# Kernel tuning notes

Hardware: AMD Instinct MI355X
Metric: run time of the kernel (lower is better)

Reference implementation:

```python
import jax, jax.numpy as jnp
import numpy as np

D_MODEL = 768
D_FF = 3072
N_BEHAVIORS = 4
EPS = 1e-12


def layer_norm(x, g, b):
    m = jnp.mean(x, axis=-1, keepdims=True)
    v = jnp.mean(jnp.square(x - m), axis=-1, keepdims=True)
    return (x - m) * jax.lax.rsqrt(v + EPS) * g + b


def setup_inputs() -> dict:
    key = jax.random.key(0)
    ks = jax.random.split(key, 8)
    B, L = 8, 2048
    s1 = 1.0 / np.sqrt(D_MODEL)
    s2 = 1.0 / np.sqrt(D_FF)
    return {
        "input_tensor": jax.random.normal(ks[0], (B, L, D_MODEL), dtype=jnp.float32),
        "type_seq": jax.random.randint(ks[1], (B, L), 0, N_BEHAVIORS + 1),
        # per-behavior FeedForward params, stacked on leading n dim
        "W1": jax.random.normal(ks[2], (N_BEHAVIORS, D_MODEL, D_FF), dtype=jnp.float32) * s1,
        "b1": jnp.zeros((N_BEHAVIORS, D_FF), dtype=jnp.float32),
        "W2": jax.random.normal(ks[3], (N_BEHAVIORS, D_FF, D_MODEL), dtype=jnp.float32) * s2,
        "b2": jnp.zeros((N_BEHAVIORS, D_MODEL), dtype=jnp.float32),
        "ln_g": jnp.ones((N_BEHAVIORS, D_MODEL), dtype=jnp.float32),
        "ln_b": jnp.zeros((N_BEHAVIORS, D_MODEL), dtype=jnp.float32),
        # outer LayerNorm params
        "out_g": jnp.ones((D_MODEL,), dtype=jnp.float32),
        "out_b": jnp.zeros((D_MODEL,), dtype=jnp.float32),
    }


def reference(input_tensor, type_seq, W1, b1, W2, b2, ln_g, ln_b, out_g, out_b):
    n = W1.shape[0]
    # run every behavior's FeedForward over the full sequence (dense over-compute)
    h = jnp.einsum('BLH,nHF->nBLF', input_tensor, W1) + b1[:, None, None, :]
    h = jax.nn.gelu(h, approximate=False)  # torch 'gelu' = exact erf form
    h = jnp.einsum('nBLF,nFH->nBLH', h, W2) + b2[:, None, None, :]
    # per-expert residual LayerNorm (FeedForward with residual=True)
    h = layer_norm(h + input_tensor[None], ln_g[:, None, None, :], ln_b[:, None, None, :])
    # prepend zeros branch (class 0 = padding) then one-hot select per token
    stacked = jnp.concatenate([jnp.zeros_like(input_tensor)[None], h], axis=0)  # [n+1,B,L,H]
    onehot = jax.nn.one_hot(type_seq, n + 1, dtype=input_tensor.dtype)  # [B,L,n+1]
    sel = jnp.einsum('nBLH,BLn->BLH', stacked, onehot)
    # dropout is identity in eval; fused residual + LayerNorm
    return layer_norm(sel + input_tensor, out_g, out_b)
```

## Files before the change

kernel.cpp:

```cpp
#include <hip/hip_runtime.h>
#include <hip/hip_bf16.h>
#include <math.h>

#define NTOK   16384
#define DM     768
#define DF     3072
#define NEXP   4

#define RBLKS  64
#define XBLKS  768
#define WBLKS  288
#define PREP_BLKS (RBLKS + XBLKS + WBLKS)
#define W2BLKS 288

typedef short bf16x8 __attribute__((ext_vector_type(8)));
typedef float f32x4  __attribute__((ext_vector_type(4)));

#define WS_CNT    0u
#define WS_BASES  256u
#define WS_POS    512u
#define WS_LIST   (512u + 65536u)
#define WS_XB     (WS_LIST + 262144u)
#define WS_W1T    (WS_XB + 25165824u)
#define WS_W2T    (WS_W1T + 18874368u)
#define WS_H1     (WS_W2T + 18874368u)
#define WS_H2     (WS_H1 + 100663296u)
#define WS_END    (WS_H2 + 25165824u)

__device__ __forceinline__ ushort f2bf(float f) {
    unsigned int v; __builtin_memcpy(&v, &f, 4);
    v = v + 0x7fffu + ((v >> 16) & 1u);
    return (ushort)(v >> 16);
}
__device__ __forceinline__ float bf2f(ushort u) {
    unsigned int v = ((unsigned int)u) << 16;
    float f; __builtin_memcpy(&f, &v, 4); return f;
}

__device__ __forceinline__ float fast_gelu(float v) {
    float y = v + 0.044715f * v * v * v;
    float e = __builtin_amdgcn_exp2f(-2.3022082f * y);
    return v * __builtin_amdgcn_rcpf(1.0f + e);
}

typedef __attribute__((address_space(1))) const void gvoid_t;
typedef __attribute__((address_space(3))) void lvoid_t;
__device__ __forceinline__ void cp16(const void* g, void* l) {
    __builtin_amdgcn_global_load_lds((gvoid_t*)g, (lvoid_t*)l, 16, 0, 0);
}

__device__ __forceinline__ int xcd_remap(int id, int T) {
    const int q = T >> 3, r = T & 7;
    const int x = id & 7, j = id >> 3;
    return (x < r ? x * (q + 1) : r * (q + 1) + (x - r) * q) + j;
}

__global__ __launch_bounds__(256) void prep_kernel(
    const int* __restrict__ type_seq, const float* __restrict__ X,
    const float* __restrict__ W1,
    int* __restrict__ cnt,
    int* __restrict__ pos_of, int* __restrict__ list,
    ushort* __restrict__ Xb, ushort* __restrict__ W1t) {
    __shared__ ushort tbuf[2][64 * 72];
    __shared__ int lcnt[NEXP];
    __shared__ int lbase[NEXP];
    const int tid = threadIdx.x;
    const int bid = blockIdx.x;

    if (bid < RBLKS) {
        if (tid < NEXP) lcnt[tid] = 0;
        __syncthreads();
        const int lane = tid & 63;
        const int t = bid * 256 + tid;
        const int k = type_seq[t];
        int my_e = -1, my_p = 0;
#pragma unroll
        for (int e = 0; e < NEXP; ++e) {
            unsigned long long m = __ballot(k == e + 1);
            int total = __popcll(m);
            int b = 0;
            if (lane == 0 && total) b = atomicAdd(&lcnt[e], total);
            b = __shfl(b, 0, 64);
            if (k == e + 1) {
                my_e = e;
                my_p = b + __popcll(m & ((1ull << lane) - 1ull));
            }
        }
        __syncthreads();
        if (tid < NEXP && lcnt[tid] > 0)
            lbase[tid] = atomicAdd(&cnt[tid], lcnt[tid]);
        __syncthreads();
        if (my_e >= 0) {
            int gp = lbase[my_e] + my_p;
            list[my_e * NTOK + gp] = t;
            pos_of[t] = gp;
        }
        return;
    }

    int id = bid - RBLKS;
    if (id < XBLKS) {
        size_t ibase = ((size_t)id * 8 * 256 + tid) * 8;
        float4 va[8], vb[8];
#pragma unroll
        for (int k = 0; k < 8; ++k) {
            va[k] = *(const float4*)(X + ibase + (size_t)k * 2048);
            vb[k] = *(const float4*)(X + ibase + (size_t)k * 2048 + 4);
        }
#pragma unroll
        for (int k = 0; k < 8; ++k) {
            ushort tmp[8];
            tmp[0] = f2bf(va[k].x); tmp[1] = f2bf(va[k].y);
            tmp[2] = f2bf(va[k].z); tmp[3] = f2bf(va[k].w);
            tmp[4] = f2bf(vb[k].x); tmp[5] = f2bf(vb[k].y);
            tmp[6] = f2bf(vb[k].z); tmp[7] = f2bf(vb[k].w);
            *(uint4*)(Xb + ibase + (size_t)k * 2048) = *(uint4*)tmp;
        }
        return;
    }
    id -= XBLKS;
    {
        const int lr = tid >> 3;
        const int lc = (tid & 7) * 8;
        float4 v[2][2];
        const int base_tt = id * 8;
        auto LOADT = [&](int tt) {
            int z = tt / 576, rr = tt % 576, bx = rr % 48, by = rr / 48;
            const float* s0 = W1 + (size_t)z * DM * DF + (size_t)(by * 64 + lr) * DF + bx * 64 + lc;
            v[0][0] = *(const float4*)s0;       v[0][1] = *(const float4*)(s0 + 4);
            const float* s1 = s0 + (size_t)32 * DF;
            v[1][0] = *(const float4*)s1;       v[1][1] = *(const float4*)(s1 + 4);
        };
        LOADT(base_tt);
#pragma unroll 1
        for (int k = 0; k < 8; ++k) {
            ushort* tb = &tbuf[k & 1][0];
#pragma unroll
            for (int q = 0; q < 2; ++q) {
                int r = lr + q * 32;
                ushort tmp[8];
                tmp[0] = f2bf(v[q][0].x); tmp[1] = f2bf(v[q][0].y);
                tmp[2] = f2bf(v[q][0].z); tmp[3] = f2bf(v[q][0].w);
                tmp[4] = f2bf(v[q][1].x); tmp[5] = f2bf(v[q][1].y);
                tmp[6] = f2bf(v[q][1].z); tmp[7] = f2bf(v[q][1].w);
                int sw = (((lc >> 3) ^ ((r >> 3) & 7)) << 3);
                *(uint4*)&tb[r * 72 + sw] = *(uint4*)tmp;
            }
            if (k < 7) LOADT(base_tt + k + 1);
            __syncthreads();
            int tt = base_tt + k;
            int z = tt / 576, rr = tt % 576, bx = rr % 48, by = rr / 48;
#pragma unroll
            for (int q = 0; q < 2; ++q) {
                int r = lr + q * 32;
                ushort tmp[8];
#pragma unroll
                for (int j = 0; j < 8; ++j)
                    tmp[j] = tb[(lc + j) * 72 +
                                ((((r >> 3) & 7) ^ (((lc + j) >> 3) & 7)) << 3) + (r & 7)];
                *(uint4*)(W1t + (size_t)z * DM * DF + (size_t)(bx * 64 + r) * DM + by * 64 + lc) = *(uint4*)tmp;
            }
        }
    }
}

__global__ __launch_bounds__(512, 4) void gemm1_kernel(
    const ushort* __restrict__ Xb, const ushort* __restrict__ W1t,
    const float* __restrict__ b1, const int* __restrict__ cnt,
    const int* __restrict__ list, ushort* __restrict__ h1,
    const float* __restrict__ W2, ushort* __restrict__ W2t) {
    __shared__ __align__(16) short As[3][4096];
    __shared__ __align__(16) short Bs[3][4096];
    const int tid = threadIdx.x;

    const int c0 = cnt[0], c1 = cnt[1], c2 = cnt[2], c3 = cnt[3];
    const int p0 = (c0 + 127) >> 7, p1 = (c1 + 127) >> 7, p2 = (c2 + 127) >> 7;
    const int mb = p0 + p1 + p2 + ((c3 + 127) >> 7);
    const int T = mb * 24;
    int id = blockIdx.y * 24 + blockIdx.x;

    if (id >= T) {
        int wid = id - T;
        if (wid >= W2BLKS) return;
        ushort* tb = (ushort*)&As[0][0];
        const int lr = tid >> 3;
        const int lc = (tid & 7) * 8;
#pragma unroll 1
        for (int k = 0; k < 8; ++k) {
            int tt = wid * 8 + k;
            int zz = tt / 576, rr = tt % 576, bx = rr % 12, by = rr / 12;
            size_t mbase = (size_t)zz * DM * DF;
            const float* s = W2 + mbase + (size_t)(by * 64 + lr) * DM + bx * 64 + lc;
            float4 v0 = *(const float4*)s;
            float4 v1 = *(const float4*)(s + 4);
            ushort tmp[8];
            tmp[0] = f2bf(v0.x); tmp[1] = f2bf(v0.y); tmp[2] = f2bf(v0.z); tmp[3] = f2bf(v0.w);
            tmp[4] = f2bf(v1.x); tmp[5] = f2bf(v1.y); tmp[6] = f2bf(v1.z); tmp[7] = f2bf(v1.w);
            int sw = (((lc >> 3) ^ ((lr >> 3) & 7)) << 3);
            __syncthreads();
            *(uint4*)&tb[lr * 72 + sw] = *(uint4*)tmp;
            __syncthreads();
            ushort o[8];
#pragma unroll
            for (int j = 0; j < 8; ++j)
                o[j] = tb[(lc + j) * 72 +
                          ((((lr >> 3) & 7) ^ (((lc + j) >> 3) & 7)) << 3) + (lr & 7)];
            *(uint4*)(W2t + mbase + (size_t)(bx * 64 + lr) * DF + by * 64 + lc) = *(uint4*)o;
        }
        return;
    }

    id = xcd_remap(id, T);
    const int y = id / 24;
    const int n0 = (id % 24) * 128;
    const int q1 = p0, q2 = p0 + p1, q3 = p0 + p1 + p2;
    const int e = (y >= q1) + (y >= q2) + (y >= q3);
    const int mstart = (e > 0) * p0 + (e > 1) * p1 + (e > 2) * p2;
    const int m0 = (y - mstart) << 7;
    const int count = (e == 0) ? c0 : ((e == 1) ? c1 : ((e == 2) ? c2 : c3));
    const int base = (e > 0) * c0 + (e > 1) * c1 + (e > 2) * c2;
    const int NK = DM / 32;

    const int wave = tid >> 6, lane = tid & 63;
    const int wm = (wave & 1) * 64, wn = (wave >> 1) * 32;
    const int lrow = lane & 15;
    const int qg = lane >> 4;

    int r0 = min(m0 + (tid >> 2), count - 1);
    int t0 = list[e * NTOK + r0];
    const int qsrc = ((tid & 3) ^ ((tid >> 3) & 3)) * 8;
    const ushort* a0 = Xb + (size_t)t0 * DM + qsrc;
    const ushort* Wb = W1t + (size_t)e * DF * DM;
    const ushort* bp0 = Wb + (size_t)(n0 + (tid >> 2)) * DM + qsrc;

    int aOff[4], bOff[2];
#pragma unroll
    for (int i = 0; i < 4; ++i) {
        int ra = wm + i * 16 + lrow;
        aOff[i] = ra * 32 + (qg ^ ((ra >> 1) & 3)) * 8;
    }
#pragma unroll
    for (int j = 0; j < 2; ++j) {
        int rb = wn + j * 16 + lrow;
        bOff[j] = rb * 32 + (qg ^ ((rb >> 1) & 3)) * 8;
    }

    f32x4 z = {0.f, 0.f, 0.f, 0.f};
    f32x4 acc[4][2];
#pragma unroll
    for (int i = 0; i < 4; ++i)
#pragma unroll
        for (int j = 0; j < 2; ++j) acc[i][j] = z;

    auto STAGE = [&](int wb) {
        cp16(a0, &As[0][0] + wb * 4096 + tid * 8);
        cp16(bp0, &Bs[0][0] + wb * 4096 + tid * 8);
        a0 += 32; bp0 += 32;
    };

    STAGE(0); STAGE(1);
    int rb = 0;
    for (int ks = 0; ks < NK; ++ks) {
        __builtin_amdgcn_sched_barrier(0);
        if (ks + 1 < NK) { asm volatile("s_waitcnt vmcnt(2)" ::: "memory"); }
        else             { asm volatile("s_waitcnt vmcnt(0)" ::: "memory"); }
        __builtin_amdgcn_s_barrier();
        __builtin_amdgcn_sched_barrier(0);
        if (ks + 2 < NK) {
            int wb = rb - 1; if (wb < 0) wb += 3;
            STAGE(wb);
        }
        const short* Ab = &As[0][0] + rb * 4096;
        const short* Bb = &Bs[0][0] + rb * 4096;
        bf16x8 av[4], bv[2];
#pragma unroll
        for (int i = 0; i < 4; ++i) av[i] = *(const bf16x8*)(Ab + aOff[i]);
#pragma unroll
        for (int j = 0; j < 2; ++j) bv[j] = *(const bf16x8*)(Bb + bOff[j]);
#pragma unroll
        for (int i = 0; i < 4; ++i)
#pragma unroll
            for (int j = 0; j < 2; ++j)
                acc[i][j] = __builtin_amdgcn_mfma_f32_16x16x32_bf16(av[i], bv[j], acc[i][j], 0, 0, 0);
        rb = (rb + 1 == 3) ? 0 : rb + 1;
    }

    float bias[2];
#pragma unroll
    for (int nt = 0; nt < 2; ++nt)
        bias[nt] = b1[e * DF + n0 + wn + nt * 16 + lrow];
#pragma unroll
    for (int mt = 0; mt < 4; ++mt) {
        int gm = m0 + wm + mt * 16 + (lane >> 4) * 4;
#pragma unroll
        for (int nt = 0; nt < 2; ++nt) {
            int gn = n0 + wn + nt * 16 + lrow;
#pragma unroll
            for (int r = 0; r < 4; ++r) {
                int i = gm + r;
                if (i < count) {
                    float v = acc[mt][nt][r] + bias[nt];
                    h1[(size_t)(base + i) * DF + gn] = f2bf(fast_gelu(v));
                }
            }
        }
    }
}

__global__ __launch_bounds__(256, 3) void gemm2_kernel(
    const ushort* __restrict__ h1, const ushort* __restrict__ W2t,
    const float* __restrict__ b2, const int* __restrict__ cnt,
    ushort* __restrict__ h2) {
    const int c0 = cnt[0], c1 = cnt[1], c2 = cnt[2], c3 = cnt[3];
    const int p0 = (c0 + 127) >> 7, p1 = (c1 + 127) >> 7, p2 = (c2 + 127) >> 7;
    const int mb = p0 + p1 + p2 + ((c3 + 127) >> 7);
    const int T = mb * 6;
    int id = blockIdx.y * 6 + blockIdx.x;
    if (id >= T) return;
    id = xcd_remap(id, T);
    const int y = id / 6;
    const int n0 = (id % 6) * 128;
    const int q1 = p0, q2 = p0 + p1, q3 = p0 + p1 + p2;
    const int e = (y >= q1) + (y >= q2) + (y >= q3);
    const int mstart = (e > 0) * p0 + (e > 1) * p1 + (e > 2) * p2;
    const int m0 = (y - mstart) << 7;
    const int count = (e == 0) ? c0 : ((e == 1) ? c1 : ((e == 2) ? c2 : c3));
    const int base = (e > 0) * c0 + (e > 1) * c1 + (e > 2) * c2;
    const int NK = DF / 32;

    __shared__ __align__(16) short As[3][4096];
    __shared__ __align__(16) short Bs[3][4096];

    const int tid = threadIdx.x;
    const int wave = tid >> 6, lane = tid & 63;
    const int wm = (wave & 1) * 64, wn = (wave >> 1) * 64;
    const int lrow = lane & 15;
    const int qg = lane >> 4;

    const int srow = tid >> 2;
    const int qsrc = ((tid & 3) ^ ((tid >> 3) & 3)) * 8;
    int r0 = min(m0 + srow, count - 1);
    int r1 = min(m0 + 64 + srow, count - 1);
    const ushort* a0 = h1 + (size_t)(base + r0) * DF + qsrc;
    const ushort* a1 = h1 + (size_t)(base + r1) * DF + qsrc;
    const ushort* Wb = W2t + (size_t)e * DM * DF;
    const ushort* bp0 = Wb + (size_t)(n0 + srow) * DF + qsrc;
    const ushort* bp1 = bp0 + (size_t)64 * DF;

    int aOff[4], bOff[4];
#pragma unroll
    for (int i = 0; i < 4; ++i) {
        int ra = wm + i * 16 + lrow;
        aOff[i] = ra * 32 + (qg ^ ((ra >> 1) & 3)) * 8;
        int rbo = wn + i * 16 + lrow;
        bOff[i] = rbo * 32 + (qg ^ ((rbo >> 1) & 3)) * 8;
    }

    f32x4 z = {0.f, 0.f, 0.f, 0.f};
    f32x4 acc[4][4];
#pragma unroll
    for (int i = 0; i < 4; ++i)
#pragma unroll
        for (int j = 0; j < 4; ++j) acc[i][j] = z;

    auto STAGE = [&](int wb) {
        cp16(a0, &As[wb][0] + tid * 8);
        cp16(a1, &As[wb][2048] + tid * 8);
        cp16(bp0, &Bs[wb][0] + tid * 8);
        cp16(bp1, &Bs[wb][2048] + tid * 8);
        a0 += 32; a1 += 32; bp0 += 32; bp1 += 32;
    };

    STAGE(0); STAGE(1);
    int rb = 0;
    for (int ks = 0; ks < NK; ++ks) {
        __builtin_amdgcn_sched_barrier(0);
        if (ks + 1 < NK) { asm volatile("s_waitcnt vmcnt(4)" ::: "memory"); }
        else             { asm volatile("s_waitcnt vmcnt(0)" ::: "memory"); }
        __builtin_amdgcn_s_barrier();
        __builtin_amdgcn_sched_barrier(0);
        if (ks + 2 < NK) {
            int wb = rb - 1; if (wb < 0) wb += 3;
            STAGE(wb);
        }
        const short* Ab = &As[rb][0];
        const short* Bb = &Bs[rb][0];
        bf16x8 av[4], bv[4];
#pragma unroll
        for (int i = 0; i < 4; ++i) av[i] = *(const bf16x8*)(Ab + aOff[i]);
#pragma unroll
        for (int j = 0; j < 4; ++j) bv[j] = *(const bf16x8*)(Bb + bOff[j]);
#pragma unroll
        for (int i = 0; i < 4; ++i)
#pragma unroll
            for (int j = 0; j < 4; ++j)
                acc[i][j] = __builtin_amdgcn_mfma_f32_16x16x32_bf16(av[i], bv[j], acc[i][j], 0, 0, 0);
        rb = (rb + 1 == 3) ? 0 : rb + 1;
    }

    float bias[4];
#pragma unroll
    for (int j = 0; j < 4; ++j)
        bias[j] = b2[e * DM + n0 + wn + j * 16 + lrow];
#pragma unroll
    for (int i = 0; i < 4; ++i) {
        int gm = m0 + wm + i * 16 + qg * 4;
#pragma unroll
        for (int j = 0; j < 4; ++j) {
            int gn = n0 + wn + j * 16 + lrow;
#pragma unroll
            for (int r = 0; r < 4; ++r) {
                int row = gm + r;
                if (row < count)
                    h2[(size_t)(base + row) * DM + gn] = f2bf(acc[i][j][r] + bias[j]);
            }
        }
    }
}

__global__ __launch_bounds__(256) void finalize_kernel(
    const float* __restrict__ X, const int* __restrict__ type_seq,
    const int* __restrict__ pos_of, const int* __restrict__ cnt,
    const ushort* __restrict__ h2,
    const float* __restrict__ ln_g, const float* __restrict__ ln_b,
    const float* __restrict__ out_g, const float* __restrict__ out_b,
    float* __restrict__ out) {
    const int tid = threadIdx.x;
    const int wave = tid >> 6, lane = tid & 63;
    const int col0 = lane * 4;
    const int c0 = cnt[0], c1 = cnt[1], c2 = cnt[2];

#pragma unroll 1
    for (int ti = 0; ti < 2; ++ti) {
        const int t = blockIdx.x * 8 + wave * 2 + ti;
        const int k = type_seq[t];

        const float* Xr = X + (size_t)t * DM;
        float4 xv[3];
#pragma unroll
        for (int j = 0; j < 3; ++j) xv[j] = *(const float4*)(Xr + col0 + j * 256);

        float rv[12];
        if (k > 0) {
            const int e = k - 1;
            const int base = (e > 0) * c0 + (e > 1) * c1 + (e > 2) * c2;
            const size_t row = (size_t)(base + pos_of[t]);
            const ushort* hr = h2 + row * DM;
            float v[12];
            float s1 = 0.f, s2 = 0.f;
#pragma unroll
            for (int j = 0; j < 3; ++j) {
                ushort4 hv = *(const ushort4*)(hr + col0 + j * 256);
                float f0 = bf2f(hv.x) + xv[j].x;
                float f1 = bf2f(hv.y) + xv[j].y;
                float f2 = bf2f(hv.z) + xv[j].z;
                float f3 = bf2f(hv.w) + xv[j].w;
                v[j * 4 + 0] = f0; v[j * 4 + 1] = f1;
                v[j * 4 + 2] = f2; v[j * 4 + 3] = f3;
                s1 += (f0 + f1) + (f2 + f3);
                s2 += (f0 * f0 + f1 * f1) + (f2 * f2 + f3 * f3);
            }
#pragma unroll
            for (int off = 32; off > 0; off >>= 1) {
                s1 += __shfl_xor(s1, off, 64);
                s2 += __shfl_xor(s2, off, 64);
            }
            float m = s1 * (1.f / DM);
            float inv = rsqrtf(s2 * (1.f / DM) - m * m + 1e-12f);
#pragma unroll
            for (int j = 0; j < 3; ++j) {
                float4 g = *(const float4*)(ln_g + e * DM + col0 + j * 256);
                float4 b = *(const float4*)(ln_b + e * DM + col0 + j * 256);
                rv[j * 4 + 0] = (v[j * 4 + 0] - m) * inv * g.x + b.x;
                rv[j * 4 + 1] = (v[j * 4 + 1] - m) * inv * g.y + b.y;
                rv[j * 4 + 2] = (v[j * 4 + 2] - m) * inv * g.z + b.z;
                rv[j * 4 + 3] = (v[j * 4 + 3] - m) * inv * g.w + b.w;
            }
        } else {
#pragma unroll
            for (int j = 0; j < 12; ++j) rv[j] = 0.f;
        }

        float w[12];
        float s1 = 0.f, s2 = 0.f;
#pragma unroll
        for (int j = 0; j < 3; ++j) {
            float f0 = rv[j * 4 + 0] + xv[j].x;
            float f1 = rv[j * 4 + 1] + xv[j].y;
            float f2 = rv[j * 4 + 2] + xv[j].z;
            float f3 = rv[j * 4 + 3] + xv[j].w;
            w[j * 4 + 0] = f0; w[j * 4 + 1] = f1;
            w[j * 4 + 2] = f2; w[j * 4 + 3] = f3;
            s1 += (f0 + f1) + (f2 + f3);
            s2 += (f0 * f0 + f1 * f1) + (f2 * f2 + f3 * f3);
        }
#pragma unroll
        for (int off = 32; off > 0; off >>= 1) {
            s1 += __shfl_xor(s1, off, 64);
            s2 += __shfl_xor(s2, off, 64);
        }
        float m = s1 * (1.f / DM);
        float inv = rsqrtf(s2 * (1.f / DM) - m * m + 1e-12f);
#pragma unroll
        for (int j = 0; j < 3; ++j) {
            float4 g = *(const float4*)(out_g + col0 + j * 256);
            float4 b = *(const float4*)(out_b + col0 + j * 256);
            float4 o;
            o.x = (w[j * 4 + 0] - m) * inv * g.x + b.x;
            o.y = (w[j * 4 + 1] - m) * inv * g.y + b.y;
            o.z = (w[j * 4 + 2] - m) * inv * g.z + b.z;
            o.w = (w[j * 4 + 3] - m) * inv * g.w + b.w;
            *(float4*)(out + (size_t)t * DM + col0 + j * 256) = o;
        }
    }
}

extern "C" void kernel_launch(void* const* d_in, const int* in_sizes, int n_in,
                              void* d_out, int out_size, void* d_ws, size_t ws_size,
                              hipStream_t stream) {
    if (ws_size < (size_t)WS_END) return;

    const float* X     = (const float*)d_in[0];
    const int*   type  = (const int*)d_in[1];
    const float* W1    = (const float*)d_in[2];
    const float* b1    = (const float*)d_in[3];
    const float* W2    = (const float*)d_in[4];
    const float* b2    = (const float*)d_in[5];
    const float* ln_g  = (const float*)d_in[6];
    const float* ln_b  = (const float*)d_in[7];
    const float* out_g = (const float*)d_in[8];
    const float* out_b = (const float*)d_in[9];
    float* out = (float*)d_out;

    char* ws = (char*)d_ws;
    int* cnt    = (int*)(ws + WS_CNT);
    int* pos_of = (int*)(ws + WS_POS);
    int* list   = (int*)(ws + WS_LIST);
    ushort* Xb  = (ushort*)(ws + WS_XB);
    ushort* W1t = (ushort*)(ws + WS_W1T);
    ushort* W2t = (ushort*)(ws + WS_W2T);
    ushort* h1  = (ushort*)(ws + WS_H1);
    ushort* h2  = (ushort*)(ws + WS_H2);

    hipMemsetAsync(cnt, 0, NEXP * sizeof(int), stream);
    prep_kernel<<<PREP_BLKS, 256, 0, stream>>>(type, X, W1,
                                               cnt, pos_of, list, Xb, W1t);
    gemm1_kernel<<<dim3(24, 144), 512, 0, stream>>>(Xb, W1t, b1, cnt, list, h1, W2, W2t);
    gemm2_kernel<<<dim3(6, 132), 256, 0, stream>>>(h1, W2t, b2, cnt, h2);
    finalize_kernel<<<NTOK / 8, 256, 0, stream>>>(X, type, pos_of, cnt, h2, ln_g, ln_b, out_g, out_b, out);
}
```

Measured before the change: 374.4 us.

## Fuse X fp32-to-bf16 conversion into gemm1 A-tile loading

Removes the standalone pass in prep that converted the whole input X to bf16 in workspace. Instead, gemm1 loads fp32 rows of X directly into registers, converts them to bf16, and writes them into the LDS A tile, while B keeps its async global-to-LDS copy. The aim is to save the extra global read and write of X and the extra prep blocks. In exchange, gemm1 reads twice the bytes for A on each N tile, routes A through registers with extra conversion work, and relies on hand-tuned waitcnt counts.

```diff
diff --git a/kernel.cpp b/kernel.cpp
--- a/kernel.cpp
+++ b/kernel.cpp
@@ -8,9 +8,8 @@
 #define NEXP   4
 
 #define RBLKS  64
-#define XBLKS  768
 #define WBLKS  288
-#define PREP_BLKS (RBLKS + XBLKS + WBLKS)
+#define PREP_BLKS (RBLKS + WBLKS)
 #define W2BLKS 288
 
 typedef short bf16x8 __attribute__((ext_vector_type(8)));
@@ -56,11 +55,10 @@
 }
 
 __global__ __launch_bounds__(256) void prep_kernel(
-    const int* __restrict__ type_seq, const float* __restrict__ X,
-    const float* __restrict__ W1,
+    const int* __restrict__ type_seq, const float* __restrict__ W1,
     int* __restrict__ cnt,
     int* __restrict__ pos_of, int* __restrict__ list,
-    ushort* __restrict__ Xb, ushort* __restrict__ W1t) {
+    ushort* __restrict__ W1t) {
     __shared__ ushort tbuf[2][64 * 72];
     __shared__ int lcnt[NEXP];
     __shared__ int lbase[NEXP];
@@ -98,28 +96,8 @@
         return;
     }
 
-    int id = bid - RBLKS;
-    if (id < XBLKS) {
-        size_t ibase = ((size_t)id * 8 * 256 + tid) * 8;
-        float4 va[8], vb[8];
-#pragma unroll
-        for (int k = 0; k < 8; ++k) {
-            va[k] = *(const float4*)(X + ibase + (size_t)k * 2048);
-            vb[k] = *(const float4*)(X + ibase + (size_t)k * 2048 + 4);
-        }
-#pragma unroll
-        for (int k = 0; k < 8; ++k) {
-            ushort tmp[8];
-            tmp[0] = f2bf(va[k].x); tmp[1] = f2bf(va[k].y);
-            tmp[2] = f2bf(va[k].z); tmp[3] = f2bf(va[k].w);
-            tmp[4] = f2bf(vb[k].x); tmp[5] = f2bf(vb[k].y);
-            tmp[6] = f2bf(vb[k].z); tmp[7] = f2bf(vb[k].w);
-            *(uint4*)(Xb + ibase + (size_t)k * 2048) = *(uint4*)tmp;
-        }
-        return;
-    }
-    id -= XBLKS;
     {
+        int id = bid - RBLKS;
         const int lr = tid >> 3;
         const int lc = (tid & 7) * 8;
         float4 v[2][2];
@@ -165,7 +143,7 @@
 }
 
 __global__ __launch_bounds__(512, 4) void gemm1_kernel(
-    const ushort* __restrict__ Xb, const ushort* __restrict__ W1t,
+    const float* __restrict__ X, const ushort* __restrict__ W1t,
     const float* __restrict__ b1, const int* __restrict__ cnt,
     const int* __restrict__ list, ushort* __restrict__ h1,
     const float* __restrict__ W2, ushort* __restrict__ W2t) {
@@ -229,7 +207,7 @@
     int r0 = min(m0 + (tid >> 2), count - 1);
     int t0 = list[e * NTOK + r0];
     const int qsrc = ((tid & 3) ^ ((tid >> 3) & 3)) * 8;
-    const ushort* a0 = Xb + (size_t)t0 * DM + qsrc;
+    const float* aX = X + (size_t)t0 * DM + qsrc;
     const ushort* Wb = W1t + (size_t)e * DF * DM;
     const ushort* bp0 = Wb + (size_t)(n0 + (tid >> 2)) * DM + qsrc;
 
@@ -241,8 +219,8 @@
     }
 #pragma unroll
     for (int j = 0; j < 2; ++j) {
-        int rb = wn + j * 16 + lrow;
-        bOff[j] = rb * 32 + (qg ^ ((rb >> 1) & 3)) * 8;
+        int rbx = wn + j * 16 + lrow;
+        bOff[j] = rbx * 32 + (qg ^ ((rbx >> 1) & 3)) * 8;
     }
 
     f32x4 z = {0.f, 0.f, 0.f, 0.f};
@@ -252,23 +230,44 @@
 #pragma unroll
         for (int j = 0; j < 2; ++j) acc[i][j] = z;
 
-    auto STAGE = [&](int wb) {
-        cp16(a0, &As[0][0] + wb * 4096 + tid * 8);
+    float4 af0, af1;
+    auto ALOAD = [&]() {
+        af0 = *(const float4*)aX; af1 = *(const float4*)(aX + 4); aX += 32;
+    };
+    auto AWRITE = [&](int wb) {
+        ushort tmp[8];
+        tmp[0] = f2bf(af0.x); tmp[1] = f2bf(af0.y); tmp[2] = f2bf(af0.z); tmp[3] = f2bf(af0.w);
+        tmp[4] = f2bf(af1.x); tmp[5] = f2bf(af1.y); tmp[6] = f2bf(af1.z); tmp[7] = f2bf(af1.w);
+        *(uint4*)(&As[0][0] + wb * 4096 + tid * 8) = *(uint4*)tmp;
+    };
+    auto BSTAGE = [&](int wb) {
         cp16(bp0, &Bs[0][0] + wb * 4096 + tid * 8);
-        a0 += 32; bp0 += 32;
+        bp0 += 32;
     };
 
-    STAGE(0); STAGE(1);
+    ALOAD();
+    BSTAGE(0);
+    asm volatile("s_waitcnt vmcnt(1)" ::: "memory");
+    AWRITE(0);
+    ALOAD();
+    BSTAGE(1);
+
     int rb = 0;
     for (int ks = 0; ks < NK; ++ks) {
         __builtin_amdgcn_sched_barrier(0);
-        if (ks + 1 < NK) { asm volatile("s_waitcnt vmcnt(2)" ::: "memory"); }
+        if (ks + 1 < NK) { asm volatile("s_waitcnt vmcnt(1)" ::: "memory"); }
         else             { asm volatile("s_waitcnt vmcnt(0)" ::: "memory"); }
+        asm volatile("s_waitcnt lgkmcnt(0)" ::: "memory");
         __builtin_amdgcn_s_barrier();
         __builtin_amdgcn_sched_barrier(0);
-        if (ks + 2 < NK) {
-            int wb = rb - 1; if (wb < 0) wb += 3;
-            STAGE(wb);
+        if (ks + 1 < NK) {
+            int wa = rb + 1; if (wa >= 3) wa -= 3;
+            AWRITE(wa);
+            if (ks + 2 < NK) {
+                ALOAD();
+                int wb = rb + 2; if (wb >= 3) wb -= 3;
+                BSTAGE(wb);
+            }
         }
         const short* Ab = &As[0][0] + rb * 4096;
         const short* Bb = &Bs[0][0] + rb * 4096;
@@ -536,16 +535,14 @@
     int* cnt    = (int*)(ws + WS_CNT);
     int* pos_of = (int*)(ws + WS_POS);
     int* list   = (int*)(ws + WS_LIST);
-    ushort* Xb  = (ushort*)(ws + WS_XB);
     ushort* W1t = (ushort*)(ws + WS_W1T);
     ushort* W2t = (ushort*)(ws + WS_W2T);
     ushort* h1  = (ushort*)(ws + WS_H1);
     ushort* h2  = (ushort*)(ws + WS_H2);
 
     hipMemsetAsync(cnt, 0, NEXP * sizeof(int), stream);
-    prep_kernel<<<PREP_BLKS, 256, 0, stream>>>(type, X, W1,
-                                               cnt, pos_of, list, Xb, W1t);
-    gemm1_kernel<<<dim3(24, 144), 512, 0, stream>>>(Xb, W1t, b1, cnt, list, h1, W2, W2t);
+    prep_kernel<<<PREP_BLKS, 256, 0, stream>>>(type, W1, cnt, pos_of, list, W1t);
+    gemm1_kernel<<<dim3(24, 144), 512, 0, stream>>>(X, W1t, b1, cnt, list, h1, W2, W2t);
     gemm2_kernel<<<dim3(6, 132), 256, 0, stream>>>(h1, W2t, b2, cnt, h2);
     finalize_kernel<<<NTOK / 8, 256, 0, stream>>>(X, type, pos_of, cnt, h2, ln_g, ln_b, out_g, out_b, out);
 }
```

Measured after the change: 401.9 us. 1.07x slower.
